# Kernel tuning notes

Hardware: AMD Instinct MI355X
Metric: run time of the kernel (lower is better)

The kernel has to match this reference:

```python
import jax, jax.numpy as jnp
import numpy as np
from jax import lax

B = 512
THRESHOLD = 0.5
CFG = [64, 64, 'M', 128, 128, 'M', 256, 256, 256, 'M', 512, 512, 512, 'M', 512, 512, 512, 'M']  # VGG16


def _conv_relu(x, w, b):
    # x: [B,C,H,W], w: [O,I,3,3] (torch OIHW layout), pad=1 stride=1
    y = lax.conv_general_dilated(x, w, (1, 1), 'SAME',
                                 dimension_numbers=('NCHW', 'OIHW', 'NCHW'))
    return jax.nn.relu(y + b[None, :, None, None])


def _maxpool2(x):
    return lax.reduce_window(x, -jnp.inf, lax.max, (1, 1, 2, 2), (1, 1, 2, 2), 'VALID')


def _features(x, ws, bs):
    i = 0
    for c in CFG:
        if c == 'M':
            x = _maxpool2(x)
        else:
            x = _conv_relu(x, ws[i], bs[i])
            i += 1
    return x  # [B,512,1,1]


def _gcn(distance):
    # Faithful translation, including the source bug: 'onetensor' is zeros_like,
    # so mask==0 everywhere and A_hat collapses to the identity.
    n = distance.shape[0]
    zero = jnp.zeros_like(distance)
    one = jnp.zeros_like(distance)  # bug in original: torch.zeros_like for onetensor
    adj = jnp.where(distance > THRESHOLD, distance, zero)
    mask = jnp.where(distance > THRESHOLD, one, zero)
    idx = lax.top_k(adj, 10)[1]                                   # [n,10]
    top10 = jnp.zeros_like(adj).at[jnp.arange(n)[:, None], idx].set(1.0)
    top10 = top10 * mask
    a_hat = top10 + jnp.eye(n, dtype=distance.dtype)
    d_inv = jnp.diag(1.0 / jnp.sum(a_hat, axis=1))
    return lax.stop_gradient(a_hat @ d_inv)                        # [n,n]


def _forward(x, target, conv_ws, conv_bs, lin1_w, lin1_b, lin2_w, lin2_b, cls_w, cls_b):
    feat = _features(x, conv_ws, conv_bs).reshape(x.shape[0], -1)  # [B,512]
    h = jax.nn.relu(feat @ lin1_w + lin1_b)                        # [B,256]
    low = h @ lin2_w + lin2_b                                      # [B,128]
    graph_pre = jax.nn.sigmoid(low @ low.T)                        # [B,B]
    graph_gt = (target[:, None] == target[None, :]).astype(jnp.float32)
    mat = _gcn(graph_pre)                                          # [B,B], detached
    out = (mat @ feat) @ cls_w + cls_b                             # [B,10]
    return out, graph_pre, graph_gt


def setup_inputs() -> dict:
    key = jax.random.key(0)
    ks = iter(jax.random.split(key, 64))
    inp = {}
    inp['x'] = jax.random.normal(next(ks), (B, 3, 32, 32), dtype=jnp.float32)
    inp['target'] = jax.random.randint(next(ks), (B,), 0, 10)
    in_c, i = 3, 0
    for c in CFG:
        if c == 'M':
            continue
        scale = 1.0 / np.sqrt(in_c * 9.0)
        inp['conv%d_w' % i] = jax.random.normal(next(ks), (c, in_c, 3, 3), dtype=jnp.float32) * scale
        inp['conv%d_b' % i] = jnp.zeros((c,), dtype=jnp.float32)
        in_c, i = c, i + 1
    inp['lin1_w'] = jax.random.normal(next(ks), (512, 256), dtype=jnp.float32) * (1.0 / np.sqrt(512.0))
    inp['lin1_b'] = jnp.zeros((256,), dtype=jnp.float32)
    inp['lin2_w'] = jax.random.normal(next(ks), (256, 128), dtype=jnp.float32) * (1.0 / np.sqrt(256.0))
    inp['lin2_b'] = jnp.zeros((128,), dtype=jnp.float32)
    inp['cls_w'] = jax.random.normal(next(ks), (512, 10), dtype=jnp.float32) * (1.0 / np.sqrt(512.0))
    inp['cls_b'] = jnp.zeros((10,), dtype=jnp.float32)
    return inp


def reference(x, target,
              conv0_w, conv0_b, conv1_w, conv1_b, conv2_w, conv2_b, conv3_w, conv3_b,
              conv4_w, conv4_b, conv5_w, conv5_b, conv6_w, conv6_b, conv7_w, conv7_b,
              conv8_w, conv8_b, conv9_w, conv9_b, conv10_w, conv10_b, conv11_w, conv11_b,
              conv12_w, conv12_b,
              lin1_w, lin1_b, lin2_w, lin2_b, cls_w, cls_b):
    ws = [conv0_w, conv1_w, conv2_w, conv3_w, conv4_w, conv5_w, conv6_w,
          conv7_w, conv8_w, conv9_w, conv10_w, conv11_w, conv12_w]
    bs = [conv0_b, conv1_b, conv2_b, conv3_b, conv4_b, conv5_b, conv6_b,
          conv7_b, conv8_b, conv9_b, conv10_b, conv11_b, conv12_b]
    return _forward(x, target, ws, bs, lin1_w, lin1_b, lin2_w, lin2_b, cls_w, cls_b)
```

## Files before the change

kernel.cpp:

```cpp
#include <hip/hip_runtime.h>

typedef unsigned short u16;
typedef __bf16 bf16x8 __attribute__((ext_vector_type(8)));
typedef float floatx4 __attribute__((ext_vector_type(4)));

__device__ inline u16 f2bf(float f) {
    unsigned int u = __float_as_uint(f);
    unsigned int r = (u + 0x7FFFu + ((u >> 16) & 1u)) >> 16;
    return (u16)r;
}
__device__ inline float bf2f(u16 h) {
    return __uint_as_float(((unsigned int)h) << 16);
}

__device__ __forceinline__ void async_copy16(u16* lds, const u16* g) {
    __builtin_amdgcn_global_load_lds(
        (const __attribute__((address_space(1))) unsigned int*)(uintptr_t)g,
        (__attribute__((address_space(3))) unsigned int*)(unsigned int)(uintptr_t)lds,
        16, 0, 0);
}

__global__ void zero_halo(u16* __restrict__ buf, int Hp, int C, int total8)
{
    int i = blockIdx.x * 256 + threadIdx.x;
    if (i >= total8) return;
    int c8 = i % (C / 8);
    int p  = i / (C / 8);
    int ring = 4 * Hp - 4;
    int h = p % ring;
    int b = p / ring;
    int y, x;
    if (h < Hp)              { y = 0;              x = h; }
    else if (h < 2 * Hp)     { y = Hp - 1;         x = h - Hp; }
    else if (h < 3 * Hp - 2) { y = h - 2 * Hp + 1; x = 0; }
    else                     { y = h - 3 * Hp + 3; x = Hp - 1; }
    uint4 z = make_uint4(0u, 0u, 0u, 0u);
    *(uint4*)(buf + ((size_t)((b * Hp + y) * Hp + x) * C) + c8 * 8) = z;
}

__global__ __launch_bounds__(256) void conv0_kernel(
    const float* __restrict__ x, const float* __restrict__ w,
    const float* __restrict__ bias, u16* __restrict__ out)
{
    __shared__ __align__(16) float xs[3][6][36];
    const int t  = threadIdx.x;
    const int b  = blockIdx.x >> 3;
    const int y0 = (blockIdx.x & 7) * 4;

    for (int i = t; i < 3 * 6 * 36; i += 256) {
        int ci  = i / 216;
        int rem = i % 216;
        int r   = rem / 36;
        int c   = rem % 36;
        int gy  = y0 - 1 + r;
        int gx  = c - 1;
        float v = 0.f;
        if ((unsigned)gy < 32u && (unsigned)gx < 32u)
            v = x[((b * 3 + ci) * 32 + gy) * 32 + gx];
        xs[ci][r][c] = v;
    }
    const int lane = t & 63;
    const int wv   = t >> 6;
    float wr[27];
    #pragma unroll
    for (int k = 0; k < 27; k++) wr[k] = w[lane * 27 + k];
    const float bz = bias[lane];
    __syncthreads();

    const int y = y0 + wv;
    u16* orow = out + ((size_t)((b * 34 + y + 1) * 34 + 1) * 64) + lane;
    for (int xg = 0; xg < 32; xg += 4) {
        float a0 = bz, a1 = bz, a2 = bz, a3 = bz;
        #pragma unroll
        for (int ci = 0; ci < 3; ci++) {
            #pragma unroll
            for (int rr = 0; rr < 3; rr++) {
                const float* row = &xs[ci][wv + rr][0];
                float4 c03 = *(const float4*)(row + xg);
                float2 c45 = *(const float2*)(row + xg + 4);
                float w0 = wr[ci * 9 + rr * 3 + 0];
                float w1 = wr[ci * 9 + rr * 3 + 1];
                float w2 = wr[ci * 9 + rr * 3 + 2];
                a0 += c03.x * w0 + c03.y * w1 + c03.z * w2;
                a1 += c03.y * w0 + c03.z * w1 + c03.w * w2;
                a2 += c03.z * w0 + c03.w * w1 + c45.x * w2;
                a3 += c03.w * w0 + c45.x * w1 + c45.y * w2;
            }
        }
        orow[(xg + 0) * 64] = f2bf(fmaxf(a0, 0.f));
        orow[(xg + 1) * 64] = f2bf(fmaxf(a1, 0.f));
        orow[(xg + 2) * 64] = f2bf(fmaxf(a2, 0.f));
        orow[(xg + 3) * 64] = f2bf(fmaxf(a3, 0.f));
    }
}

__global__ void repack_w(const float* __restrict__ w, u16* __restrict__ wt,
                         int Cin, int total)
{
    int i = blockIdx.x * 256 + threadIdx.x;
    if (i >= total) return;
    int ci = i % Cin;
    int rest = i / Cin;
    int s = rest % 9;
    int co = rest / 9;
    wt[i] = f2bf(w[(co * Cin + ci) * 9 + s]);
}

__global__ void repack_lin(const float* __restrict__ w, u16* __restrict__ wt,
                           int K, int N, int total)
{
    int i = blockIdx.x * 256 + threadIdx.x;
    if (i >= total) return;
    int n = i % N, k = i / N;
    wt[(size_t)n * K + k] = f2bf(w[(size_t)k * N + n]);
}

template <int BN>
__global__ __launch_bounds__(256) void conv_gemm(
    const u16* __restrict__ in, const u16* __restrict__ wt,
    const float* __restrict__ bias, u16* __restrict__ out,
    float* __restrict__ partial, size_t pstride,
    int H, int Cin, int Cout, int logHW, int logW, int splitN,
    int outPad, int poolMode)
{
    constexpr int BM = 128, BK = 64;
    constexpr int NT   = BN / 32;
    constexpr int NB_A = 4;
    constexpr int NB_B = BN / 32;
    __shared__ u16 As[BM * BK];
    __shared__ u16 Bs[BN * BK];

    const int Nblocks = Cout / BN;
    const int per = gridDim.x >> 3;
    const int bid = (blockIdx.x & 7) * per + (blockIdx.x >> 3);
    const int sp   = bid % splitN;
    const int tile = bid / splitN;
    const int m0 = (tile / Nblocks) * BM;
    const int n0 = (tile % Nblocks) * BN;

    const int t    = threadIdx.x;
    const int lane = t & 63;
    const int wave = t >> 6;
    const int quad = lane >> 4;
    const int l16  = lane & 15;
    const int wm   = wave >> 1;
    const int wn   = wave & 1;
    const int W    = H;
    const int Wp   = H + 2;
    const int HW   = 1 << logHW;
    const int col8 = t & 7;
    const int r0   = t >> 3;
    const int scol = col8 ^ (r0 & 7);

    const int CinB = Cin * 2;

    int vA[NB_A];
    #pragma unroll
    for (int j = 0; j < NB_A; j++) {
        int m  = m0 + r0 + 32 * j;
        int b  = m >> logHW;
        int rm = m & (HW - 1);
        int y  = rm >> logW;
        int xx = rm & (W - 1);
        vA[j] = ((b * Wp + y + 1) * Wp + xx + 1) * CinB + scol * 16;
    }
    int vB[NB_B];
    #pragma unroll
    for (int j = 0; j < NB_B; j++)
        vB[j] = (n0 + r0 + 32 * j) * 9 * CinB + scol * 16;

    const int logKB = (Cin == 64) ? 0 : (Cin == 128) ? 1 : (Cin == 256) ? 2 : 3;
    const int KB  = 1 << logKB;
    const int T   = 9 * KB;
    const int len = T / splitN;
    const int it0 = sp * len;

    int s0 = it0 >> logKB;
    int c3 = s0 - (s0 / 3) * 3;
    int ta = ((s0 / 3 - 1) * Wp + (c3 - 1)) * CinB;
    int kb = (it0 & (KB - 1)) * 128;
    int tb = it0 * 128;

    u16* const ldsA = As + t * 8;
    u16* const ldsB = Bs + t * 8;
    const char* const inB = (const char*)in;
    const char* const wtB = (const char*)wt;

    floatx4 acc[4][NT];
    #pragma unroll
    for (int i = 0; i < 4; i++)
        #pragma unroll
        for (int j = 0; j < NT; j++)
            acc[i][j] = (floatx4){0.f, 0.f, 0.f, 0.f};

    const int sw = (l16 & 7) * 8;

    for (int it = 0; it < len; it++) {
        const int ua = ta + kb;
        #pragma unroll
        for (int j = 0; j < NB_A; j++)
            async_copy16(ldsA + j * 2048, (const u16*)(inB + (ua + vA[j])));
        #pragma unroll
        for (int j = 0; j < NB_B; j++)
            async_copy16(ldsB + j * 2048, (const u16*)(wtB + (tb + vB[j])));
        __syncthreads();
        #pragma unroll
        for (int kk = 0; kk < BK; kk += 32) {
            bf16x8 af[4], bfv[NT];
            int cbo = kk + quad * 8;
            #pragma unroll
            for (int mt = 0; mt < 4; mt++)
                af[mt] = *(const bf16x8*)(As + (wm * 64 + mt * 16 + l16) * 64 + (cbo ^ sw));
            #pragma unroll
            for (int nt = 0; nt < NT; nt++)
                bfv[nt] = *(const bf16x8*)(Bs + (wn * (BN / 2) + nt * 16 + l16) * 64 + (cbo ^ sw));
            #pragma unroll
            for (int mt = 0; mt < 4; mt++)
                #pragma unroll
                for (int nt = 0; nt < NT; nt++)
                    acc[mt][nt] = __builtin_amdgcn_mfma_f32_16x16x32_bf16(
                        af[mt], bfv[nt], acc[mt][nt], 0, 0, 0);
        }
        __syncthreads();
        tb += 128;
        kb += 128;
        if (kb == CinB) {
            kb = 0;
            ta += (c3 == 2) ? (Wp - 2) * CinB : CinB;
            c3 = (c3 == 2) ? 0 : c3 + 1;
        }
    }

    if (splitN > 1) {
        float* pout = partial + (size_t)sp * pstride;
        #pragma unroll
        for (int mt = 0; mt < 4; mt++)
            #pragma unroll
            for (int nt = 0; nt < NT; nt++)
                #pragma unroll
                for (int r = 0; r < 4; r++) {
                    int mg = m0 + wm * 64 + mt * 16 + quad * 4 + r;
                    int ng = n0 + wn * (BN / 2) + nt * 16 + l16;
                    pout[(size_t)mg * Cout + ng] = acc[mt][nt][r];
                }
        return;
    }

    if (poolMode) {
        const int Hpo = (H >> 1) + 2;
        #pragma unroll
        for (int nt = 0; nt < NT; nt++) {
            int ng = n0 + wn * (BN / 2) + nt * 16 + l16;
            float bz = bias[ng];
            if (logW == 5) {
                #pragma unroll
                for (int mt = 0; mt < 2; mt++)
                    #pragma unroll
                    for (int rp = 0; rp < 2; rp++) {
                        float v = fmaxf(
                            fmaxf(acc[mt][nt][2 * rp], acc[mt][nt][2 * rp + 1]),
                            fmaxf(acc[mt + 2][nt][2 * rp], acc[mt + 2][nt][2 * rp + 1]));
                        int m1 = m0 + wm * 64 + mt * 16 + quad * 4 + 2 * rp;
                        int b  = m1 >> logHW;
                        int rm = m1 & (HW - 1);
                        int yp = (rm >> logW) >> 1;
                        int xp = (rm & (W - 1)) >> 1;
                        out[(size_t)((b * Hpo + yp + 1) * Hpo + xp + 1) * Cout + ng] =
                            f2bf(fmaxf(v + bz, 0.f));
                    }
            } else if (logW == 4) {
                #pragma unroll
                for (int mtp = 0; mtp < 2; mtp++)
                    #pragma unroll
                    for (int rp = 0; rp < 2; rp++) {
                        int mt = 2 * mtp;
                        float v = fmaxf(
                            fmaxf(acc[mt][nt][2 * rp], acc[mt][nt][2 * rp + 1]),
                            fmaxf(acc[mt + 1][nt][2 * rp], acc[mt + 1][nt][2 * rp + 1]));
                        int m1 = m0 + wm * 64 + mt * 16 + quad * 4 + 2 * rp;
                        int b  = m1 >> logHW;
                        int rm = m1 & (HW - 1);
                        int yp = (rm >> logW) >> 1;
                        int xp = (rm & (W - 1)) >> 1;
                        out[(size_t)((b * Hpo + yp + 1) * Hpo + xp + 1) * Cout + ng] =
                            f2bf(fmaxf(v + bz, 0.f));
                    }
            } else if (logW == 3) {
                #pragma unroll
                for (int mt = 0; mt < 4; mt++)
                    #pragma unroll
                    for (int rp = 0; rp < 2; rp++) {
                        float a = fmaxf(acc[mt][nt][2 * rp], acc[mt][nt][2 * rp + 1]);
                        float p = __shfl_xor(a, 32, 64);
                        float v = fmaxf(a, p);
                        if (quad < 2) {
                            int m1 = m0 + wm * 64 + mt * 16 + quad * 4 + 2 * rp;
                            int b  = m1 >> logHW;
                            int rm = m1 & (HW - 1);
                            int yp = (rm >> logW) >> 1;
                            int xp = (rm & (W - 1)) >> 1;
                            out[(size_t)((b * Hpo + yp + 1) * Hpo + xp + 1) * Cout + ng] =
                                f2bf(fmaxf(v + bz, 0.f));
                        }
                    }
            } else {
                #pragma unroll
                for (int mt = 0; mt < 4; mt++)
                    #pragma unroll
                    for (int rp = 0; rp < 2; rp++) {
                        float a = fmaxf(acc[mt][nt][2 * rp], acc[mt][nt][2 * rp + 1]);
                        float p = __shfl_xor(a, 16, 64);
                        float v = fmaxf(a, p);
                        if (!(quad & 1)) {
                            int m1 = m0 + wm * 64 + mt * 16 + quad * 4 + 2 * rp;
                            int b  = m1 >> logHW;
                            int rm = m1 & (HW - 1);
                            int yp = (rm >> logW) >> 1;
                            int xp = (rm & (W - 1)) >> 1;
                            out[(size_t)((b * Hpo + yp + 1) * Hpo + xp + 1) * Cout + ng] =
                                f2bf(fmaxf(v + bz, 0.f));
                        }
                    }
            }
        }
        return;
    }

    #pragma unroll
    for (int mt = 0; mt < 4; mt++) {
        #pragma unroll
        for (int r = 0; r < 4; r++) {
            int mg = m0 + wm * 64 + mt * 16 + quad * 4 + r;
            size_t obase;
            if (outPad) {
                int b  = mg >> logHW;
                int rm = mg & (HW - 1);
                int y  = rm >> logW;
                int xx = rm & (W - 1);
                obase = (size_t)((b * Wp + y + 1) * Wp + xx + 1) * Cout;
            } else {
                obase = (size_t)mg * Cout;
            }
            #pragma unroll
            for (int nt = 0; nt < NT; nt++) {
                int ng = n0 + wn * (BN / 2) + nt * 16 + l16;
                float v = acc[mt][nt][r] + bias[ng];
                out[obase + ng] = f2bf(fmaxf(v, 0.f));
            }
        }
    }
}

__global__ void reduce_split(const float* __restrict__ partial,
                             const float* __restrict__ bias, u16* __restrict__ out,
                             int MN, int C, int logC, int splitN, size_t pstride,
                             int H, int logHW, int logW, int outPad)
{
    int i4 = (blockIdx.x * 256 + threadIdx.x) * 4;
    if (i4 >= MN) return;
    float4 s = *(const float4*)(partial + i4);
    for (int sp = 1; sp < splitN; sp++) {
        float4 p = *(const float4*)(partial + (size_t)sp * pstride + i4);
        s.x += p.x; s.y += p.y; s.z += p.z; s.w += p.w;
    }
    int n = i4 & (C - 1);
    int m = i4 >> logC;
    size_t obase;
    if (outPad) {
        int Wp = H + 2;
        int b  = m >> logHW;
        int rm = m & ((1 << logHW) - 1);
        int y  = rm >> logW;
        int xx = rm & (H - 1);
        obase = (size_t)((b * Wp + y + 1) * Wp + xx + 1) * C;
    } else {
        obase = (size_t)m * C;
    }
    ushort4 o;
    o.x = f2bf(fmaxf(s.x + bias[n + 0], 0.f));
    o.y = f2bf(fmaxf(s.y + bias[n + 1], 0.f));
    o.z = f2bf(fmaxf(s.z + bias[n + 2], 0.f));
    o.w = f2bf(fmaxf(s.w + bias[n + 3], 0.f));
    *(ushort4*)(out + obase + n) = o;
}

__global__ void reduce_pool(const float* __restrict__ partial,
                            const float* __restrict__ bias, u16* __restrict__ out,
                            int total4, int C, int splitN, size_t pstride,
                            int H, int outPad)
{
    int idx = blockIdx.x * 256 + threadIdx.x;
    if (idx >= total4) return;
    int c4 = idx % (C / 4);
    int p  = idx / (C / 4);
    int Ho = H >> 1;
    int xp = p % Ho; p /= Ho;
    int yp = p % Ho;
    int b  = p / Ho;
    int n  = c4 * 4;
    float4 best;
    bool first = true;
    #pragma unroll
    for (int dy = 0; dy < 2; dy++)
        #pragma unroll
        for (int dx = 0; dx < 2; dx++) {
            int m = (b * H + 2 * yp + dy) * H + 2 * xp + dx;
            const float* q = partial + (size_t)m * C + n;
            float4 s = *(const float4*)q;
            for (int sp = 1; sp < splitN; sp++) {
                float4 pp = *(const float4*)(q + (size_t)sp * pstride);
                s.x += pp.x; s.y += pp.y; s.z += pp.z; s.w += pp.w;
            }
            if (first) { best = s; first = false; }
            else {
                best.x = fmaxf(best.x, s.x); best.y = fmaxf(best.y, s.y);
                best.z = fmaxf(best.z, s.z); best.w = fmaxf(best.w, s.w);
            }
        }
    size_t obase;
    if (outPad) {
        int Hpo = Ho + 2;
        obase = (size_t)((b * Hpo + yp + 1) * Hpo + xp + 1) * C;
    } else {
        obase = (size_t)((b * Ho + yp) * Ho + xp) * C;
    }
    ushort4 o;
    o.x = f2bf(fmaxf(best.x + bias[n + 0], 0.f));
    o.y = f2bf(fmaxf(best.y + bias[n + 1], 0.f));
    o.z = f2bf(fmaxf(best.z + bias[n + 2], 0.f));
    o.w = f2bf(fmaxf(best.w + bias[n + 3], 0.f));
    *(ushort4*)(out + obase + n) = o;
}

template <bool RELU, bool OUTBF>
__global__ __launch_bounds__(256) void gemm64(
    const u16* __restrict__ A, const u16* __restrict__ Bt,
    const float* __restrict__ bias, void* __restrict__ outv,
    int M, int N, int K)
{
    constexpr int LDP = 72;
    __shared__ u16 As[64 * LDP];
    __shared__ u16 Bs[64 * LDP];

    const int nb = N >> 6;
    const int m0 = (blockIdx.x / nb) * 64;
    const int n0 = (blockIdx.x % nb) * 64;
    const int t = threadIdx.x, lane = t & 63, wave = t >> 6;
    const int quad = lane >> 4, l16 = lane & 15;
    const int wm = wave >> 1, wn = wave & 1;
    const int col8 = t & 7, r0 = t >> 3;

    floatx4 acc[2][2];
    #pragma unroll
    for (int i = 0; i < 2; i++)
        #pragma unroll
        for (int j = 0; j < 2; j++)
            acc[i][j] = (floatx4){0.f, 0.f, 0.f, 0.f};

    for (int kb = 0; kb < K; kb += 64) {
        #pragma unroll
        for (int j = 0; j < 2; j++) {
            int row = r0 + 32 * j;
            *(uint4*)(As + row * LDP + col8 * 8) =
                *(const uint4*)(A + (size_t)(m0 + row) * K + kb + col8 * 8);
            *(uint4*)(Bs + row * LDP + col8 * 8) =
                *(const uint4*)(Bt + (size_t)(n0 + row) * K + kb + col8 * 8);
        }
        __syncthreads();
        #pragma unroll
        for (int kk = 0; kk < 64; kk += 32) {
            bf16x8 af[2], bfv[2];
            #pragma unroll
            for (int mt = 0; mt < 2; mt++)
                af[mt] = *(const bf16x8*)(As + (wm * 32 + mt * 16 + l16) * LDP + kk + quad * 8);
            #pragma unroll
            for (int nt = 0; nt < 2; nt++)
                bfv[nt] = *(const bf16x8*)(Bs + (wn * 32 + nt * 16 + l16) * LDP + kk + quad * 8);
            #pragma unroll
            for (int mt = 0; mt < 2; mt++)
                #pragma unroll
                for (int nt = 0; nt < 2; nt++)
                    acc[mt][nt] = __builtin_amdgcn_mfma_f32_16x16x32_bf16(
                        af[mt], bfv[nt], acc[mt][nt], 0, 0, 0);
        }
        __syncthreads();
    }
    #pragma unroll
    for (int mt = 0; mt < 2; mt++) {
        #pragma unroll
        for (int nt = 0; nt < 2; nt++) {
            #pragma unroll
            for (int r = 0; r < 4; r++) {
                int mg = m0 + wm * 32 + mt * 16 + quad * 4 + r;
                int ng = n0 + wn * 32 + nt * 16 + l16;
                float v = acc[mt][nt][r] + bias[ng];
                if (RELU) v = fmaxf(v, 0.f);
                if (OUTBF) ((u16*)outv)[(size_t)mg * N + ng] = f2bf(v);
                else       ((float*)outv)[(size_t)mg * N + ng] = v;
            }
        }
    }
}

__global__ __launch_bounds__(256) void graph_tile(
    const float* __restrict__ low, const int* __restrict__ target,
    float* __restrict__ gpre, float* __restrict__ ggt)
{
    __shared__ float Al[64 * 132];
    __shared__ float Bl[128 * 68];
    const int t = threadIdx.x;
    const int gr0 = (blockIdx.x >> 3) * 64;
    const int gc0 = (blockIdx.x & 7) * 64;

    #pragma unroll
    for (int j = 0; j < 32; j++) {
        int flat = t + 256 * j;
        int k = flat & 127;
        int rc = flat >> 7;
        Al[rc * 132 + k] = low[(size_t)(gr0 + rc) * 128 + k];
        Bl[k * 68 + rc]  = low[(size_t)(gc0 + rc) * 128 + k];
    }
    __syncthreads();

    const int tx = t & 15, ty = t >> 4;
    float acc[4][4];
    #pragma unroll
    for (int r = 0; r < 4; r++)
        #pragma unroll
        for (int c = 0; c < 4; c++) acc[r][c] = 0.f;

    for (int k = 0; k < 128; k++) {
        float a[4], b[4];
        #pragma unroll
        for (int r = 0; r < 4; r++) a[r] = Al[(ty * 4 + r) * 132 + k];
        #pragma unroll
        for (int c = 0; c < 4; c++) b[c] = Bl[k * 68 + tx * 4 + c];
        #pragma unroll
        for (int r = 0; r < 4; r++)
            #pragma unroll
            for (int c = 0; c < 4; c++) acc[r][c] += a[r] * b[c];
    }
    #pragma unroll
    for (int r = 0; r < 4; r++) {
        int row = gr0 + ty * 4 + r;
        int tr  = target[row];
        float4 gp, gg;
        float* pp = (float*)&gp;
        float* gg_ = (float*)&gg;
        #pragma unroll
        for (int c = 0; c < 4; c++) {
            pp[c]  = 1.f / (1.f + __expf(-acc[r][c]));
            gg_[c] = (tr == target[gc0 + tx * 4 + c]) ? 1.f : 0.f;
        }
        *(float4*)(gpre + (size_t)row * 512 + gc0 + tx * 4) = gp;
        *(float4*)(ggt  + (size_t)row * 512 + gc0 + tx * 4) = gg;
    }
}

__global__ __launch_bounds__(256) void cls_kernel(
    const u16* __restrict__ feat, const float* __restrict__ w,
    const float* __restrict__ bias, float* __restrict__ out)
{
    __shared__ float ws[5120];
    const int t = threadIdx.x;
    for (int i = t; i < 5120; i += 256) ws[i] = w[i];
    __syncthreads();
    const int lane = t & 63;
    const int row  = blockIdx.x * 4 + (t >> 6);
    float a[10];
    #pragma unroll
    for (int j = 0; j < 10; j++) a[j] = 0.f;
    #pragma unroll
    for (int i = 0; i < 8; i++) {
        int k = i * 64 + lane;
        float f = bf2f(feat[(size_t)row * 512 + k]);
        #pragma unroll
        for (int j = 0; j < 10; j++) a[j] += f * ws[k * 10 + j];
    }
    #pragma unroll
    for (int j = 0; j < 10; j++)
        #pragma unroll
        for (int off = 32; off > 0; off >>= 1)
            a[j] += __shfl_down(a[j], off, 64);
    if (lane == 0) {
        #pragma unroll
        for (int j = 0; j < 10; j++) out[row * 10 + j] = a[j] + bias[j];
    }
}

extern "C" void kernel_launch(void* const* d_in, const int* in_sizes, int n_in,
                              void* d_out, int out_size, void* d_ws, size_t ws_size,
                              hipStream_t stream)
{
    const float* x      = (const float*)d_in[0];
    const int*   target = (const int*)d_in[1];
    const float* conv_w[13];
    const float* conv_b[13];
    for (int i = 0; i < 13; i++) {
        conv_w[i] = (const float*)d_in[2 + 2 * i];
        conv_b[i] = (const float*)d_in[3 + 2 * i];
    }
    const float* lin1_w = (const float*)d_in[28];
    const float* lin1_b = (const float*)d_in[29];
    const float* lin2_w = (const float*)d_in[30];
    const float* lin2_b = (const float*)d_in[31];
    const float* cls_w  = (const float*)d_in[32];
    const float* cls_b  = (const float*)d_in[33];
    float* out = (float*)d_out;

    static const int cin_arr[13]  = {3, 64, 64, 128, 128, 256, 256, 256, 512, 512, 512, 512, 512};
    static const int cout_arr[13] = {64, 64, 128, 128, 256, 256, 256, 512, 512, 512, 512, 512, 512};

    char* ws = (char*)d_ws;
    size_t off = 0;
    const size_t R0SZ = (size_t)512 * 34 * 34 * 64 * 2;
    const size_t R1SZ = (size_t)512 * 34 * 34 * 64 * 2;
    char* R0raw = ws + off; off += R0SZ;
    char* R1raw = ws + off; off += R1SZ;
    u16* R0 = (u16*)R0raw;
    u16* R1 = (u16*)R1raw;
    float* PA = (float*)(R0raw + 20971520);
    float* PB = (float*)(R1raw + 20971520);
    u16* wt[13];
    for (int i = 1; i < 13; i++) {
        wt[i] = (u16*)(ws + off);
        off += (size_t)cout_arr[i] * 9 * cin_arr[i] * 2;
    }
    u16* wtl1 = (u16*)(ws + off); off += (size_t)256 * 512 * 2;
    u16* wtl2 = (u16*)(ws + off); off += (size_t)128 * 256 * 2;
    u16* hbuf = (u16*)(ws + off); off += (size_t)512 * 256 * 2;
    float* lowbuf = (float*)(ws + off); off += (size_t)512 * 128 * 4;

    for (int i = 1; i < 13; i++) {
        int total = cout_arr[i] * 9 * cin_arr[i];
        repack_w<<<(total + 255) / 256, 256, 0, stream>>>(conv_w[i], wt[i], cin_arr[i], total);
    }
    repack_lin<<<(512 * 256) / 256, 256, 0, stream>>>(lin1_w, wtl1, 512, 256, 512 * 256);
    repack_lin<<<(256 * 128) / 256, 256, 0, stream>>>(lin2_w, wtl2, 256, 128, 256 * 128);

    auto zh = [&](u16* buf, int Hp, int C) {
        int total8 = 512 * (4 * Hp - 4) * (C / 8);
        zero_halo<<<(total8 + 255) / 256, 256, 0, stream>>>(buf, Hp, C, total8);
    };
    auto launch_conv = [&](int li, int Hl, int bn, u16* inb, u16* outb, float* part,
                           int splitN, int outPad, int poolMode) {
        int Cin = cin_arr[li], Cout = cout_arr[li];
        int M = 512 * Hl * Hl;
        int logW = __builtin_ctz(Hl);
        int logHW = 2 * logW;
        size_t pstride = (size_t)M * Cout;
        int grid = (M / 128) * (Cout / bn) * splitN;
        if (bn == 128) {
            conv_gemm<128><<<grid, 256, 0, stream>>>(
                inb, wt[li], conv_b[li], outb, part, pstride,
                Hl, Cin, Cout, logHW, logW, splitN, outPad, poolMode);
        } else {
            conv_gemm<64><<<grid, 256, 0, stream>>>(
                inb, wt[li], conv_b[li], outb, part, pstride,
                Hl, Cin, Cout, logHW, logW, splitN, outPad, poolMode);
        }
    };
    auto launch_reduce = [&](int li, int Hl, u16* outb, float* part, int splitN, int outPad) {
        int Cout = cout_arr[li];
        int M = 512 * Hl * Hl;
        int logW = __builtin_ctz(Hl);
        size_t pstride = (size_t)M * Cout;
        int MN = M * Cout;
        reduce_split<<<(MN / 4 + 255) / 256, 256, 0, stream>>>(
            part, conv_b[li], outb, MN, Cout, __builtin_ctz(Cout),
            splitN, pstride, Hl, 2 * logW, logW, outPad);
    };
    auto launch_reduce_pool = [&](int li, int Hl, u16* outb, float* part, int splitN, int outPad) {
        int Cout = cout_arr[li];
        int M = 512 * Hl * Hl;
        size_t pstride = (size_t)M * Cout;
        int total4 = 512 * (Hl / 2) * (Hl / 2) * Cout / 4;
        reduce_pool<<<(total4 + 255) / 256, 256, 0, stream>>>(
            part, conv_b[li], outb, total4, Cout, splitN, pstride, Hl, outPad);
    };

    zh(R0, 34, 64);
    conv0_kernel<<<512 * 8, 256, 0, stream>>>(x, conv_w[0], conv_b[0], R0);

    zh(R1, 18, 64);
    launch_conv(1, 32, 64, R0, R1, nullptr, 1, 0, 1);
    zh(R0, 18, 128);
    launch_conv(2, 16, 128, R1, R0, nullptr, 1, 1, 0);
    zh(R1, 10, 128);
    launch_conv(3, 16, 128, R0, R1, nullptr, 1, 0, 1);
    zh(R0, 10, 256);
    launch_conv(4, 8, 128, R1, R0, nullptr, 1, 1, 0);
    zh(R1, 10, 256);
    launch_conv(5, 8, 128, R0, R1, nullptr, 1, 1, 0);
    zh(R0, 6, 256);
    launch_conv(6, 8, 128, R1, R0, nullptr, 1, 0, 1);
    zh(R1, 6, 512);
    launch_conv(7, 4, 128, R0, R1, PB, 2, 1, 0);
    launch_reduce(7, 4, R1, PB, 2, 1);
    zh(R0, 6, 512);
    launch_conv(8, 4, 128, R1, R0, PA, 2, 1, 0);
    launch_reduce(8, 4, R0, PA, 2, 1);
    zh(R1, 4, 512);
    launch_conv(9, 4, 128, R0, R1, PB, 2, 0, 0);
    launch_reduce_pool(9, 4, R1, PB, 2, 1);
    zh(R0, 4, 512);
    launch_conv(10, 2, 64, R1, R0, PA, 4, 1, 0);
    launch_reduce(10, 2, R0, PA, 4, 1);
    zh(R1, 4, 512);
    launch_conv(11, 2, 64, R0, R1, PB, 4, 1, 0);
    launch_reduce(11, 2, R1, PB, 4, 1);
    launch_conv(12, 2, 64, R1, R0, PA, 4, 0, 0);
    launch_reduce_pool(12, 2, R0, PA, 4, 0);

    u16* feat = R0;
    gemm64<true, true><<<(512 / 64) * (256 / 64), 256, 0, stream>>>(
        feat, wtl1, lin1_b, hbuf, 512, 256, 512);
    gemm64<false, false><<<(512 / 64) * (128 / 64), 256, 0, stream>>>(
        hbuf, wtl2, lin2_b, lowbuf, 512, 128, 256);
    graph_tile<<<64, 256, 0, stream>>>(lowbuf, target, out + 5120, out + 5120 + 262144);
    cls_kernel<<<128, 256, 0, stream>>>(feat, cls_w, cls_b, out);
}
```

Baseline: 825.5 us.

## Add 256-row conv tile for first layer, merge weight repacks, simplify epilogues

Measured after the change: 822.2 us. Within noise of the previous version (-0.4%).

```diff
diff --git a/kernel.cpp b/kernel.cpp
--- a/kernel.cpp
+++ b/kernel.cpp
@@ -5,9 +5,7 @@
 typedef float floatx4 __attribute__((ext_vector_type(4)));
 
 __device__ inline u16 f2bf(float f) {
-    unsigned int u = __float_as_uint(f);
-    unsigned int r = (u + 0x7FFFu + ((u >> 16) & 1u)) >> 16;
-    return (u16)r;
+    return __builtin_bit_cast(u16, (__bf16)f);
 }
 __device__ inline float bf2f(u16 h) {
     return __uint_as_float(((unsigned int)h) << 16);
@@ -94,28 +92,41 @@
     }
 }
 
-__global__ void repack_w(const float* __restrict__ w, u16* __restrict__ wt,
-                         int Cin, int total)
-{
-    int i = blockIdx.x * 256 + threadIdx.x;
-    if (i >= total) return;
-    int ci = i % Cin;
-    int rest = i / Cin;
-    int s = rest % 9;
-    int co = rest / 9;
-    wt[i] = f2bf(w[(co * Cin + ci) * 9 + s]);
-}
-
-__global__ void repack_lin(const float* __restrict__ w, u16* __restrict__ wt,
-                           int K, int N, int total)
-{
-    int i = blockIdx.x * 256 + threadIdx.x;
-    if (i >= total) return;
-    int n = i % N, k = i / N;
-    wt[(size_t)n * K + k] = f2bf(w[(size_t)k * N + n]);
-}
-
-template <int BN>
+struct RepackArgs {
+    const float* src[14];
+    u16* dst[14];
+    int p1[14];
+    int p2[14];
+    int total[14];
+    int startBlk[15];
+    int nseg;
+};
+
+__global__ void repack_all(RepackArgs a)
+{
+    int blk = blockIdx.x;
+    int s = 0;
+    #pragma unroll 1
+    while (s + 1 < a.nseg && blk >= a.startBlk[s + 1]) s++;
+    int i = (blk - a.startBlk[s]) * 256 + threadIdx.x;
+    if (i >= a.total[s]) return;
+    const float* src = a.src[s];
+    u16* dst = a.dst[s];
+    if (a.p2[s] == 0) {
+        int Cin = a.p1[s];
+        int ci = i % Cin;
+        int rest = i / Cin;
+        int sh = rest % 9;
+        int co = rest / 9;
+        dst[i] = f2bf(src[(co * Cin + ci) * 9 + sh]);
+    } else {
+        int N = a.p2[s], K = a.p1[s];
+        int n = i % N, k = i / N;
+        dst[(size_t)n * K + k] = f2bf(src[(size_t)k * N + n]);
+    }
+}
+
+template <int BM, int BN>
 __global__ __launch_bounds__(256) void conv_gemm(
     const u16* __restrict__ in, const u16* __restrict__ wt,
     const float* __restrict__ bias, u16* __restrict__ out,
@@ -123,9 +134,10 @@
     int H, int Cin, int Cout, int logHW, int logW, int splitN,
     int outPad, int poolMode)
 {
-    constexpr int BM = 128, BK = 64;
-    constexpr int NT   = BN / 32;
-    constexpr int NB_A = 4;
+    constexpr int BK = 64;
+    constexpr int WC = (BM == 256) ? BN : (BN / 2);
+    constexpr int NT = WC / 16;
+    constexpr int NB_A = BM / 32;
     constexpr int NB_B = BN / 32;
     __shared__ u16 As[BM * BK];
     __shared__ u16 Bs[BN * BK];
@@ -143,8 +155,8 @@
     const int wave = t >> 6;
     const int quad = lane >> 4;
     const int l16  = lane & 15;
-    const int wm   = wave >> 1;
-    const int wn   = wave & 1;
+    const int wm   = (BM == 256) ? wave : (wave >> 1);
+    const int wn   = (BM == 256) ? 0 : (wave & 1);
     const int W    = H;
     const int Wp   = H + 2;
     const int HW   = 1 << logHW;
@@ -213,7 +225,7 @@
                 af[mt] = *(const bf16x8*)(As + (wm * 64 + mt * 16 + l16) * 64 + (cbo ^ sw));
             #pragma unroll
             for (int nt = 0; nt < NT; nt++)
-                bfv[nt] = *(const bf16x8*)(Bs + (wn * (BN / 2) + nt * 16 + l16) * 64 + (cbo ^ sw));
+                bfv[nt] = *(const bf16x8*)(Bs + (wn * WC + nt * 16 + l16) * 64 + (cbo ^ sw));
             #pragma unroll
             for (int mt = 0; mt < 4; mt++)
                 #pragma unroll
@@ -231,97 +243,88 @@
         }
     }
 
+    const int ngb = n0 + wn * WC + l16;
+
     if (splitN > 1) {
         float* pout = partial + (size_t)sp * pstride;
         #pragma unroll
         for (int mt = 0; mt < 4; mt++)
             #pragma unroll
-            for (int nt = 0; nt < NT; nt++)
+            for (int r = 0; r < 4; r++) {
+                int mg = m0 + wm * 64 + mt * 16 + quad * 4 + r;
+                float* op = pout + (size_t)mg * Cout + ngb;
                 #pragma unroll
-                for (int r = 0; r < 4; r++) {
-                    int mg = m0 + wm * 64 + mt * 16 + quad * 4 + r;
-                    int ng = n0 + wn * (BN / 2) + nt * 16 + l16;
-                    pout[(size_t)mg * Cout + ng] = acc[mt][nt][r];
-                }
+                for (int nt = 0; nt < NT; nt++)
+                    op[nt * 16] = acc[mt][nt][r];
+            }
         return;
     }
+
+    float bzv[NT];
+    #pragma unroll
+    for (int nt = 0; nt < NT; nt++) bzv[nt] = bias[ngb + nt * 16];
 
     if (poolMode) {
         const int Hpo = (H >> 1) + 2;
-        #pragma unroll
-        for (int nt = 0; nt < NT; nt++) {
-            int ng = n0 + wn * (BN / 2) + nt * 16 + l16;
-            float bz = bias[ng];
-            if (logW == 5) {
+        if (logW == 5) {
+            #pragma unroll
+            for (int mt = 0; mt < 2; mt++)
                 #pragma unroll
-                for (int mt = 0; mt < 2; mt++)
+                for (int rp = 0; rp < 2; rp++) {
+                    int m1 = m0 + wm * 64 + mt * 16 + quad * 4 + 2 * rp;
+                    int b  = m1 >> logHW;
+                    int rm = m1 & (HW - 1);
+                    int yp = (rm >> logW) >> 1;
+                    int xp = (rm & (W - 1)) >> 1;
+                    u16* op = out + (size_t)((b * Hpo + yp + 1) * Hpo + xp + 1) * Cout + ngb;
                     #pragma unroll
-                    for (int rp = 0; rp < 2; rp++) {
+                    for (int nt = 0; nt < NT; nt++) {
                         float v = fmaxf(
                             fmaxf(acc[mt][nt][2 * rp], acc[mt][nt][2 * rp + 1]),
                             fmaxf(acc[mt + 2][nt][2 * rp], acc[mt + 2][nt][2 * rp + 1]));
-                        int m1 = m0 + wm * 64 + mt * 16 + quad * 4 + 2 * rp;
-                        int b  = m1 >> logHW;
-                        int rm = m1 & (HW - 1);
-                        int yp = (rm >> logW) >> 1;
-                        int xp = (rm & (W - 1)) >> 1;
-                        out[(size_t)((b * Hpo + yp + 1) * Hpo + xp + 1) * Cout + ng] =
-                            f2bf(fmaxf(v + bz, 0.f));
+                        op[nt * 16] = f2bf(fmaxf(v + bzv[nt], 0.f));
                     }
-            } else if (logW == 4) {
+                }
+        } else if (logW == 4) {
+            #pragma unroll
+            for (int mtp = 0; mtp < 2; mtp++)
                 #pragma unroll
-                for (int mtp = 0; mtp < 2; mtp++)
+                for (int rp = 0; rp < 2; rp++) {
+                    int mt = 2 * mtp;
+                    int m1 = m0 + wm * 64 + mt * 16 + quad * 4 + 2 * rp;
+                    int b  = m1 >> logHW;
+                    int rm = m1 & (HW - 1);
+                    int yp = (rm >> logW) >> 1;
+                    int xp = (rm & (W - 1)) >> 1;
+                    u16* op = out + (size_t)((b * Hpo + yp + 1) * Hpo + xp + 1) * Cout + ngb;
                     #pragma unroll
-                    for (int rp = 0; rp < 2; rp++) {
-                        int mt = 2 * mtp;
+                    for (int nt = 0; nt < NT; nt++) {
                         float v = fmaxf(
                             fmaxf(acc[mt][nt][2 * rp], acc[mt][nt][2 * rp + 1]),
                             fmaxf(acc[mt + 1][nt][2 * rp], acc[mt + 1][nt][2 * rp + 1]));
-                        int m1 = m0 + wm * 64 + mt * 16 + quad * 4 + 2 * rp;
-                        int b  = m1 >> logHW;
-                        int rm = m1 & (HW - 1);
-                        int yp = (rm >> logW) >> 1;
-                        int xp = (rm & (W - 1)) >> 1;
-                        out[(size_t)((b * Hpo + yp + 1) * Hpo + xp + 1) * Cout + ng] =
-                            f2bf(fmaxf(v + bz, 0.f));
+                        op[nt * 16] = f2bf(fmaxf(v + bzv[nt], 0.f));
                     }
-            } else if (logW == 3) {
+                }
+        } else {
+            #pragma unroll
+            for (int mt = 0; mt < 4; mt++)
                 #pragma unroll
-                for (int mt = 0; mt < 4; mt++)
+                for (int rp = 0; rp < 2; rp++) {
+                    int m1 = m0 + wm * 64 + mt * 16 + quad * 4 + 2 * rp;
+                    int b  = m1 >> logHW;
+                    int rm = m1 & (HW - 1);
+                    int yp = (rm >> logW) >> 1;
+                    int xp = (rm & (W - 1)) >> 1;
+                    u16* op = out + (size_t)((b * Hpo + yp + 1) * Hpo + xp + 1) * Cout + ngb;
                     #pragma unroll
-                    for (int rp = 0; rp < 2; rp++) {
+                    for (int nt = 0; nt < NT; nt++) {
                         float a = fmaxf(acc[mt][nt][2 * rp], acc[mt][nt][2 * rp + 1]);
                         float p = __shfl_xor(a, 32, 64);
                         float v = fmaxf(a, p);
-                        if (quad < 2) {
-                            int m1 = m0 + wm * 64 + mt * 16 + quad * 4 + 2 * rp;
-                            int b  = m1 >> logHW;
-                            int rm = m1 & (HW - 1);
-                            int yp = (rm >> logW) >> 1;
-                            int xp = (rm & (W - 1)) >> 1;
-                            out[(size_t)((b * Hpo + yp + 1) * Hpo + xp + 1) * Cout + ng] =
-                                f2bf(fmaxf(v + bz, 0.f));
-                        }
+                        if (quad < 2)
+                            op[nt * 16] = f2bf(fmaxf(v + bzv[nt], 0.f));
                     }
-            } else {
-                #pragma unroll
-                for (int mt = 0; mt < 4; mt++)
-                    #pragma unroll
-                    for (int rp = 0; rp < 2; rp++) {
-                        float a = fmaxf(acc[mt][nt][2 * rp], acc[mt][nt][2 * rp + 1]);
-                        float p = __shfl_xor(a, 16, 64);
-                        float v = fmaxf(a, p);
-                        if (!(quad & 1)) {
-                            int m1 = m0 + wm * 64 + mt * 16 + quad * 4 + 2 * rp;
-                            int b  = m1 >> logHW;
-                            int rm = m1 & (HW - 1);
-                            int yp = (rm >> logW) >> 1;
-                            int xp = (rm & (W - 1)) >> 1;
-                            out[(size_t)((b * Hpo + yp + 1) * Hpo + xp + 1) * Cout + ng] =
-                                f2bf(fmaxf(v + bz, 0.f));
-                        }
-                    }
-            }
+                }
         }
         return;
     }
@@ -341,12 +344,10 @@
             } else {
                 obase = (size_t)mg * Cout;
             }
-            #pragma unroll
-            for (int nt = 0; nt < NT; nt++) {
-                int ng = n0 + wn * (BN / 2) + nt * 16 + l16;
-                float v = acc[mt][nt][r] + bias[ng];
-                out[obase + ng] = f2bf(fmaxf(v, 0.f));
-            }
+            u16* op = out + obase + ngb;
+            #pragma unroll
+            for (int nt = 0; nt < NT; nt++)
+                op[nt * 16] = f2bf(fmaxf(acc[mt][nt][r] + bzv[nt], 0.f));
         }
     }
 }
@@ -631,31 +632,49 @@
     u16* hbuf = (u16*)(ws + off); off += (size_t)512 * 256 * 2;
     float* lowbuf = (float*)(ws + off); off += (size_t)512 * 128 * 4;
 
+    RepackArgs ra;
+    int nb = 0, blk = 0;
+    ra.startBlk[0] = 0;
     for (int i = 1; i < 13; i++) {
-        int total = cout_arr[i] * 9 * cin_arr[i];
-        repack_w<<<(total + 255) / 256, 256, 0, stream>>>(conv_w[i], wt[i], cin_arr[i], total);
-    }
-    repack_lin<<<(512 * 256) / 256, 256, 0, stream>>>(lin1_w, wtl1, 512, 256, 512 * 256);
-    repack_lin<<<(256 * 128) / 256, 256, 0, stream>>>(lin2_w, wtl2, 256, 128, 256 * 128);
+        ra.src[nb] = conv_w[i];
+        ra.dst[nb] = wt[i];
+        ra.p1[nb] = cin_arr[i];
+        ra.p2[nb] = 0;
+        ra.total[nb] = cout_arr[i] * 9 * cin_arr[i];
+        blk += (ra.total[nb] + 255) / 256;
+        nb++; ra.startBlk[nb] = blk;
+    }
+    ra.src[nb] = lin1_w; ra.dst[nb] = wtl1; ra.p1[nb] = 512; ra.p2[nb] = 256;
+    ra.total[nb] = 512 * 256; blk += (512 * 256 + 255) / 256;
+    nb++; ra.startBlk[nb] = blk;
+    ra.src[nb] = lin2_w; ra.dst[nb] = wtl2; ra.p1[nb] = 256; ra.p2[nb] = 128;
+    ra.total[nb] = 256 * 128; blk += (256 * 128 + 255) / 256;
+    nb++; ra.startBlk[nb] = blk;
+    ra.nseg = nb;
+    repack_all<<<blk, 256, 0, stream>>>(ra);
 
     auto zh = [&](u16* buf, int Hp, int C) {
         int total8 = 512 * (4 * Hp - 4) * (C / 8);
         zero_halo<<<(total8 + 255) / 256, 256, 0, stream>>>(buf, Hp, C, total8);
     };
-    auto launch_conv = [&](int li, int Hl, int bn, u16* inb, u16* outb, float* part,
-                           int splitN, int outPad, int poolMode) {
+    auto launch_conv = [&](int li, int Hl, int bm, int bn, u16* inb, u16* outb,
+                           float* part, int splitN, int outPad, int poolMode) {
         int Cin = cin_arr[li], Cout = cout_arr[li];
         int M = 512 * Hl * Hl;
         int logW = __builtin_ctz(Hl);
         int logHW = 2 * logW;
         size_t pstride = (size_t)M * Cout;
-        int grid = (M / 128) * (Cout / bn) * splitN;
-        if (bn == 128) {
-            conv_gemm<128><<<grid, 256, 0, stream>>>(
+        int grid = (M / bm) * (Cout / bn) * splitN;
+        if (bm == 256) {
+            conv_gemm<256, 64><<<grid, 256, 0, stream>>>(
+                inb, wt[li], conv_b[li], outb, part, pstride,
+                Hl, Cin, Cout, logHW, logW, splitN, outPad, poolMode);
+        } else if (bn == 128) {
+            conv_gemm<128, 128><<<grid, 256, 0, stream>>>(
                 inb, wt[li], conv_b[li], outb, part, pstride,
                 Hl, Cin, Cout, logHW, logW, splitN, outPad, poolMode);
         } else {
-            conv_gemm<64><<<grid, 256, 0, stream>>>(
+            conv_gemm<128, 64><<<grid, 256, 0, stream>>>(
                 inb, wt[li], conv_b[li], outb, part, pstride,
                 Hl, Cin, Cout, logHW, logW, splitN, outPad, poolMode);
         }
@@ -683,33 +702,33 @@
     conv0_kernel<<<512 * 8, 256, 0, stream>>>(x, conv_w[0], conv_b[0], R0);
 
     zh(R1, 18, 64);
-    launch_conv(1, 32, 64, R0, R1, nullptr, 1, 0, 1);
+    launch_conv(1, 32, 256, 64, R0, R1, nullptr, 1, 0, 1);
     zh(R0, 18, 128);
-    launch_conv(2, 16, 128, R1, R0, nullptr, 1, 1, 0);
+    launch_conv(2, 16, 128, 128, R1, R0, nullptr, 1, 1, 0);
     zh(R1, 10, 128);
-    launch_conv(3, 16, 128, R0, R1, nullptr, 1, 0, 1);
+    launch_conv(3, 16, 128, 128, R0, R1, nullptr, 1, 0, 1);
     zh(R0, 10, 256);
-    launch_conv(4, 8, 128, R1, R0, nullptr, 1, 1, 0);
+    launch_conv(4, 8, 128, 128, R1, R0, nullptr, 1, 1, 0);
     zh(R1, 10, 256);
-    launch_conv(5, 8, 128, R0, R1, nullptr, 1, 1, 0);
+    launch_conv(5, 8, 128, 128, R0, R1, nullptr, 1, 1, 0);
     zh(R0, 6, 256);
-    launch_conv(6, 8, 128, R1, R0, nullptr, 1, 0, 1);
+    launch_conv(6, 8, 128, 128, R1, R0, nullptr, 1, 0, 1);
     zh(R1, 6, 512);
-    launch_conv(7, 4, 128, R0, R1, PB, 2, 1, 0);
+    launch_conv(7, 4, 128, 128, R0, R1, PB, 2, 1, 0);
     launch_reduce(7, 4, R1, PB, 2, 1);
     zh(R0, 6, 512);
-    launch_conv(8, 4, 128, R1, R0, PA, 2, 1, 0);
+    launch_conv(8, 4, 128, 128, R1, R0, PA, 2, 1, 0);
     launch_reduce(8, 4, R0, PA, 2, 1);
     zh(R1, 4, 512);
-    launch_conv(9, 4, 128, R0, R1, PB, 2, 0, 0);
+    launch_conv(9, 4, 128, 128, R0, R1, PB, 2, 0, 0);
     launch_reduce_pool(9, 4, R1, PB, 2, 1);
     zh(R0, 4, 512);
-    launch_conv(10, 2, 64, R1, R0, PA, 4, 1, 0);
+    launch_conv(10, 2, 128, 64, R1, R0, PA, 4, 1, 0);
     launch_reduce(10, 2, R0, PA, 4, 1);
     zh(R1, 4, 512);
-    launch_conv(11, 2, 64, R0, R1, PB, 4, 1, 0);
+    launch_conv(11, 2, 128, 64, R0, R1, PB, 4, 1, 0);
     launch_reduce(11, 2, R1, PB, 4, 1);
-    launch_conv(12, 2, 64, R1, R0, PA, 4, 0, 0);
+    launch_conv(12, 2, 128, 64, R1, R0, PA, 4, 0, 0);
     launch_reduce_pool(12, 2, R0, PA, 4, 0);
 
     u16* feat = R0;
```
